# Kernel tuning notes

Measured on AMD Instinct MI355X. Metric: run time of the kernel, lower is better.

Reference implementation:

```python
import jax, jax.numpy as jnp
import numpy as np

NUM_CLASSES = 1000
NUM_NEIGHBOURS = 200
SIGMA = 10.0
GAUSS_CONST = 1.0 / (2.0 * SIGMA ** 2)


def setup_inputs() -> dict:
    key = jax.random.key(0)
    k1, k2, k3 = jax.random.split(key, 3)
    B, D, C = 512, 512, 100000
    features = jax.random.normal(k1, (B, D), dtype=jnp.float32)
    centres = jax.random.normal(k2, (C, D), dtype=jnp.float32)
    centre_labels = jax.random.randint(k3, (C,), 0, NUM_CLASSES)
    weight = jnp.zeros((C,), dtype=jnp.float32)
    return {"features": features, "centres": centres,
            "centre_labels": centre_labels, "weight": weight}


def _knn(features, centres, k):
    # squared euclidean distances [B, C] without materializing [B, C, D]
    f2 = jnp.sum(features * features, axis=1, keepdims=True)      # [B,1]
    c2 = jnp.sum(centres * centres, axis=1)                        # [C]
    d2 = f2 + c2[None, :] - 2.0 * features @ centres.T             # [B,C]
    _, idx = jax.lax.top_k(-d2, k)                                 # smallest k
    return idx                                                     # [B,k]


def reference(features, centres, centre_labels, weight):
    B = features.shape[0]
    K = NUM_NEIGHBOURS
    nbr = _knn(features, centres, K)                               # [B,K] int
    gathered = centres[nbr]                                        # [B,K,D]
    d2 = jnp.sum((features[:, None, :] - gathered) ** 2, axis=-1)  # [B,K]
    kernel_weights = jnp.exp(weight)                               # [C]
    d = jnp.exp(-d2 * GAUSS_CONST) * kernel_weights[nbr]           # [B,K]
    nbr_labels = centre_labels[nbr]                                # [B,K]
    rows = jnp.arange(B)[:, None]
    p = jnp.zeros((B, NUM_CLASSES), dtype=d.dtype).at[rows, nbr_labels].add(d)
    p = jnp.where(p == 0, 1e-10, p)
    p = p / jnp.sum(p, axis=1, keepdims=True)
    return jnp.log(p)
```

## Files before the change

kernel.cpp:

```cpp
#include <hip/hip_runtime.h>
#include <hip/hip_fp16.h>
#include <math.h>
#include <stdint.h>

#define D_DIM    512
#define NCLS     1000
#define KSEL     200
#define NBINS    1024
#define CAND_MAX 2048
#define GCONST   0.005
#define MARGIN   2.0f

typedef short s8v __attribute__((ext_vector_type(8)));
typedef float f4v __attribute__((ext_vector_type(4)));

#define GLOAD_LDS16(gp, lp) __builtin_amdgcn_global_load_lds( \
    (const __attribute__((address_space(1))) void*)(gp),      \
    (__attribute__((address_space(3))) void*)(lp), 16, 0, 0)

static __device__ __forceinline__ unsigned short f2bf(float x) {
    unsigned u = __float_as_uint(x);
    return (unsigned short)((u + 0x7FFFu + ((u >> 16) & 1u)) >> 16);
}

__global__ __launch_bounds__(256)
void convertF(const float* __restrict__ F, unsigned short* __restrict__ Fb,
              float* __restrict__ f2)
{
    __shared__ float red[256];
    const int r = blockIdx.x, t = threadIdx.x;
    float2 v = *(const float2*)(F + (size_t)r * D_DIM + t * 2);
    ushort2 o; o.x = f2bf(v.x); o.y = f2bf(v.y);
    *(ushort2*)(Fb + (size_t)r * D_DIM + t * 2) = o;
    red[t] = v.x * v.x + v.y * v.y;
    __syncthreads();
    for (int off = 128; off > 0; off >>= 1) {
        if (t < off) red[t] += red[t + off];
        __syncthreads();
    }
    if (t == 0) f2[r] = red[0];
}

__global__ __launch_bounds__(256)
void mfma_gemm(const unsigned short* __restrict__ Fb,
               const float* __restrict__ C,
               float* __restrict__ c2g,
               __half* __restrict__ Sm, int N)
{
    __shared__ short smem[2 * 128 * 64];
    short* As = smem;
    short* Bs = smem + 128 * 64;
    const int t    = threadIdx.x;
    const int lane = t & 63;
    const int w    = t >> 6;
    const int wm   = w >> 1, wn = w & 1;
    const int m0   = blockIdx.x * 128;
    const int n0   = blockIdx.y * 128;
    const int lrow = lane >> 3;
    const int oct  = (lane & 7) ^ lrow;
    const int quad = lane >> 4;
    const int col  = lane & 15;

    f4v acc[4][4];
#pragma unroll
    for (int i = 0; i < 4; ++i)
#pragma unroll
        for (int j = 0; j < 4; ++j) acc[i][j] = (f4v){0.f, 0.f, 0.f, 0.f};

    float  c2part[4] = {0.f, 0.f, 0.f, 0.f};
    float4 ra[4], rb[4];

#pragma unroll
    for (int cc = 0; cc < 4; ++cc) {
        int row = (w * 4 + cc) * 8 + lrow;
        int rg  = n0 + row; rg = rg < N ? rg : N - 1;
        const float* gp = C + (size_t)rg * D_DIM + oct * 8;
        ra[cc] = *(const float4*)gp;
        rb[cc] = *(const float4*)(gp + 4);
    }

    for (int k0 = 0; k0 < D_DIM; k0 += 64) {
        __syncthreads();
#pragma unroll
        for (int cc = 0; cc < 4; ++cc) {
            int ch = w * 4 + cc;
            GLOAD_LDS16(Fb + (size_t)(m0 + ch * 8 + lrow) * D_DIM + k0 + oct * 8,
                        &As[ch * 512]);
        }
#pragma unroll
        for (int cc = 0; cc < 4; ++cc) {
            int row = (w * 4 + cc) * 8 + lrow;
            float4 va = ra[cc], vb = rb[cc];
            c2part[cc] += va.x*va.x + va.y*va.y + va.z*va.z + va.w*va.w
                        + vb.x*vb.x + vb.y*vb.y + vb.z*vb.z + vb.w*vb.w;
            uint4 o;
            o.x = (unsigned)f2bf(va.x) | ((unsigned)f2bf(va.y) << 16);
            o.y = (unsigned)f2bf(va.z) | ((unsigned)f2bf(va.w) << 16);
            o.z = (unsigned)f2bf(vb.x) | ((unsigned)f2bf(vb.y) << 16);
            o.w = (unsigned)f2bf(vb.z) | ((unsigned)f2bf(vb.w) << 16);
            *(uint4*)&Bs[row * 64 + (lane & 7) * 8] = o;
        }
        __syncthreads();

        if (k0 + 64 < D_DIM) {
#pragma unroll
            for (int cc = 0; cc < 4; ++cc) {
                int row = (w * 4 + cc) * 8 + lrow;
                int rg  = n0 + row; rg = rg < N ? rg : N - 1;
                const float* gp = C + (size_t)rg * D_DIM + (k0 + 64) + oct * 8;
                ra[cc] = *(const float4*)gp;
                rb[cc] = *(const float4*)(gp + 4);
            }
        }

#pragma unroll
        for (int kk = 0; kk < 2; ++kk) {
            s8v a[4], b[4];
#pragma unroll
            for (int i = 0; i < 4; ++i) {
                int row  = wm * 64 + i * 16 + col;
                int slot = (kk * 4 + quad) ^ (col & 7);
                a[i] = *(s8v*)&As[row * 64 + slot * 8];
            }
#pragma unroll
            for (int j = 0; j < 4; ++j) {
                int row  = wn * 64 + j * 16 + col;
                int slot = (kk * 4 + quad) ^ (col & 7);
                b[j] = *(s8v*)&Bs[row * 64 + slot * 8];
            }
#pragma unroll
            for (int i = 0; i < 4; ++i)
#pragma unroll
                for (int j = 0; j < 4; ++j)
                    acc[i][j] = __builtin_amdgcn_mfma_f32_16x16x32_bf16(
                        a[i], b[j], acc[i][j], 0, 0, 0);
        }
    }

#pragma unroll
    for (int cc = 0; cc < 4; ++cc) {
        float s = c2part[cc];
        s += __shfl_xor(s, 1, 64);
        s += __shfl_xor(s, 2, 64);
        s += __shfl_xor(s, 4, 64);
        int row = (w * 4 + cc) * 8 + lrow;
        if (m0 == 0 && (lane & 7) == 0 && (n0 + row) < N)
            c2g[n0 + row] = s;
    }

    __syncthreads();
    __half* Cs = (__half*)smem;
#pragma unroll
    for (int i = 0; i < 4; ++i) {
#pragma unroll
        for (int j = 0; j < 4; ++j) {
#pragma unroll
            for (int v = 0; v < 4; ++v) {
                int ml = wm * 64 + i * 16 + quad * 4 + v;
                int nl = wn * 64 + j * 16 + col;
                int slot = ((nl >> 3) ^ (ml & 7));
                Cs[ml * 128 + slot * 8 + (nl & 7)] = __float2half(acc[i][j][v]);
            }
        }
    }
    __syncthreads();
#pragma unroll
    for (int it = 0; it < 8; ++it) {
        int idx = it * 256 + t;
        int row = idx >> 4;
        int o8  = idx & 15;
        int n   = n0 + o8 * 8;
        const __half* src = &Cs[row * 128 + ((o8 ^ (row & 7)) * 8)];
        __half* dst = Sm + (size_t)(m0 + row) * N + n;
        if (n + 7 < N) {
            *(uint4*)dst = *(const uint4*)src;
        } else if (n < N) {
            for (int e = 0; e < 8 && n + e < N; ++e) dst[e] = src[e];
        }
    }
}

__global__ __launch_bounds__(1024)
void fused_select(const __half* __restrict__ Sm, const float* __restrict__ f2,
                  const float* __restrict__ c2,
                  const float* __restrict__ F, const float* __restrict__ C,
                  const int* __restrict__ labels, const float* __restrict__ weight,
                  float* __restrict__ out, int N)
{
    __shared__ unsigned hist[NBINS];
    __shared__ float    fs[D_DIM];
    __shared__ int      idxs[CAND_MAX];
    __shared__ double   dists[CAND_MAX];
    __shared__ float    p[NCLS];
    __shared__ float    red[1024];
    __shared__ unsigned scanbuf[256];
    __shared__ float    sT;
    __shared__ unsigned scnt;

    const int r = blockIdx.x, t = threadIdx.x;
    for (int b = t; b < NBINS; b += 1024) hist[b] = 0u;
    for (int c = t; c < NCLS; c += 1024) p[c] = 0.f;
    for (int k = t; k < D_DIM; k += 1024) fs[k] = F[(size_t)r * D_DIM + k];
    if (t == 0) { sT = 1e30f; scnt = 0u; }
    __syncthreads();

    const float fr = f2[r];
    const __half* srow = Sm + (size_t)r * N;

    for (int j = t * 8; j < N; j += 8192) {
        uint4 sv = *(const uint4*)(srow + j);
        float4 ca = *(const float4*)(c2 + j);
        float4 cb = *(const float4*)(c2 + j + 4);
        float2 s0 = __half22float2(*(__half2*)&sv.x);
        float2 s1 = __half22float2(*(__half2*)&sv.y);
        float2 s2 = __half22float2(*(__half2*)&sv.z);
        float2 s3 = __half22float2(*(__half2*)&sv.w);
        float d2v[8] = { fr + ca.x - 2.f * s0.x, fr + ca.y - 2.f * s0.y,
                         fr + ca.z - 2.f * s1.x, fr + ca.w - 2.f * s1.y,
                         fr + cb.x - 2.f * s2.x, fr + cb.y - 2.f * s2.y,
                         fr + cb.z - 2.f * s3.x, fr + cb.w - 2.f * s3.y };
#pragma unroll
        for (int e = 0; e < 8; ++e) {
            int b = (int)(d2v[e] * 0.5f);
            b = b < 0 ? 0 : (b > NBINS - 1 ? NBINS - 1 : b);
            atomicAdd(&hist[b], 1u);
        }
    }
    __syncthreads();

    if (t < 256) {
        unsigned loc[NBINS / 256];
        unsigned s = 0;
#pragma unroll
        for (int i = 0; i < NBINS / 256; ++i) {
            loc[i] = hist[t * (NBINS / 256) + i];
            s += loc[i];
        }
        scanbuf[t] = s;
        __syncthreads();
        unsigned pre = 0;
        for (int u = 0; u < t; ++u) pre += scanbuf[u];
        if (pre < KSEL && pre + s >= KSEL) {
            unsigned cum = pre;
            int b = NBINS - 1;
#pragma unroll
            for (int i = 0; i < NBINS / 256; ++i) {
                cum += loc[i];
                if (cum >= KSEL) { b = t * (NBINS / 256) + i; break; }
            }
            sT = 2.0f * (float)(b + 1) + MARGIN;
        }
    } else {
        __syncthreads();
    }
    __syncthreads();
    const float Tr = sT;

    for (int j = t * 8; j < N; j += 8192) {
        uint4 sv = *(const uint4*)(srow + j);
        float4 ca = *(const float4*)(c2 + j);
        float4 cb = *(const float4*)(c2 + j + 4);
        float2 s0 = __half22float2(*(__half2*)&sv.x);
        float2 s1 = __half22float2(*(__half2*)&sv.y);
        float2 s2 = __half22float2(*(__half2*)&sv.z);
        float2 s3 = __half22float2(*(__half2*)&sv.w);
        float d2v[8] = { fr + ca.x - 2.f * s0.x, fr + ca.y - 2.f * s0.y,
                         fr + ca.z - 2.f * s1.x, fr + ca.w - 2.f * s1.y,
                         fr + cb.x - 2.f * s2.x, fr + cb.y - 2.f * s2.y,
                         fr + cb.z - 2.f * s3.x, fr + cb.w - 2.f * s3.y };
#pragma unroll
        for (int e = 0; e < 8; ++e) {
            if (d2v[e] <= Tr) {
                unsigned pos = atomicAdd(&scnt, 1u);
                if (pos < CAND_MAX) idxs[pos] = j + e;
            }
        }
    }
    __syncthreads();
    int Nc = (int)scnt;
    if (Nc > CAND_MAX) Nc = CAND_MAX;

    {
        const int wv = t >> 6, lane = t & 63;
        for (int i = wv; i < Nc; i += 16) {
            int ci = idxs[i];
            const float* cp = C + (size_t)ci * D_DIM;
            float4 a  = *(const float4*)(cp + lane * 8);
            float4 b  = *(const float4*)(cp + lane * 8 + 4);
            float4 fa = *(const float4*)(fs + lane * 8);
            float4 fb = *(const float4*)(fs + lane * 8 + 4);
            double d0 = (double)fa.x - (double)a.x;
            double d1 = (double)fa.y - (double)a.y;
            double d2 = (double)fa.z - (double)a.z;
            double d3 = (double)fa.w - (double)a.w;
            double d4 = (double)fb.x - (double)b.x;
            double d5 = (double)fb.y - (double)b.y;
            double d6 = (double)fb.z - (double)b.z;
            double d7 = (double)fb.w - (double)b.w;
            double acc = d0*d0 + d1*d1 + d2*d2 + d3*d3
                       + d4*d4 + d5*d5 + d6*d6 + d7*d7;
#pragma unroll
            for (int off = 32; off > 0; off >>= 1)
                acc += __shfl_down(acc, off, 64);
            if (lane == 0) dists[i] = acc;
        }
    }
    __syncthreads();

    int ksel = KSEL < Nc ? KSEL : Nc;
    for (int i = t; i < Nc; i += 1024) {
        double di = dists[i];
        int    ii = idxs[i];
        int rank = 0;
        for (int j = 0; j < Nc; ++j) {
            double dj = dists[j];
            rank += (dj < di) || (dj == di && idxs[j] < ii);
        }
        if (rank < ksel) {
            double wgt = exp(-di * GCONST) * exp((double)weight[ii]);
            atomicAdd(&p[labels[ii]], (float)wgt);
        }
    }
    __syncthreads();

    float s = 0.f;
    for (int c = t; c < NCLS; c += 1024) {
        float v = p[c];
        if (v == 0.f) v = 1e-10f;
        p[c] = v;
        s += v;
    }
    red[t] = s;
    __syncthreads();
    for (int o = 512; o > 0; o >>= 1) {
        if (t < o) red[t] += red[t + o];
        __syncthreads();
    }
    float total = red[0];
    for (int c = t; c < NCLS; c += 1024)
        out[(size_t)r * NCLS + c] = logf(p[c] / total);
}

extern "C" void kernel_launch(void* const* d_in, const int* in_sizes, int n_in,
                              void* d_out, int out_size, void* d_ws, size_t ws_size,
                              hipStream_t stream)
{
    const float* features = (const float*)d_in[0];
    const float* centres  = (const float*)d_in[1];
    const int*   labels   = (const int*)d_in[2];
    const float* weight   = (const float*)d_in[3];
    const int B = in_sizes[0] / D_DIM;
    const int N = in_sizes[2];
    float* out = (float*)d_out;

    uint8_t* w = (uint8_t*)d_ws;
    size_t off = 0;
    auto alloc = [&](size_t bytes) -> uint8_t* {
        uint8_t* ptr = w + off;
        off = (off + bytes + 255) & ~(size_t)255;
        return ptr;
    };
    float*          f2 = (float*)alloc((size_t)B * 4);
    float*          c2 = (float*)alloc((size_t)N * 4);
    unsigned short* Fb = (unsigned short*)alloc((size_t)B * D_DIM * 2);
    __half*         Sm = (__half*)alloc((size_t)B * N * 2);
    (void)ws_size;

    convertF<<<B, 256, 0, stream>>>(features, Fb, f2);

    dim3 ggrid(B / 128, (N + 127) / 128);
    mfma_gemm<<<ggrid, 256, 0, stream>>>(Fb, centres, c2, Sm, N);

    fused_select<<<B, 1024, 0, stream>>>(Sm, f2, c2, features, centres,
                                         labels, weight, out, N);
}
```

Baseline: 490.8 us.

## Pre-convert centres to bf16 once and replicate select histogram bins

When the workspace is large enough, a separate kernel converts all centres to bf16 and computes their squared norms once. The GEMM then loads bf16 tiles directly into LDS with global_load_lds, where before every M-block reread fp32 centres and converted them in registers. The fallback fused GEMM now uses the packed v_cvt_pk_bf16 instruction. The select kernel spreads each histogram bin over four replicas to reduce LDS atomic contention, at the cost of an extra 100MB bf16 write/read and more shared memory.

```diff
diff --git a/kernel.cpp b/kernel.cpp
--- a/kernel.cpp
+++ b/kernel.cpp
@@ -7,6 +7,7 @@
 #define NCLS     1000
 #define KSEL     200
 #define NBINS    1024
+#define HREP     4
 #define CAND_MAX 2048
 #define GCONST   0.005
 #define MARGIN   2.0f
@@ -21,6 +22,12 @@
 static __device__ __forceinline__ unsigned short f2bf(float x) {
     unsigned u = __float_as_uint(x);
     return (unsigned short)((u + 0x7FFFu + ((u >> 16) & 1u)) >> 16);
+}
+
+static __device__ __forceinline__ unsigned cvt_pk_bf16(float lo, float hi) {
+    unsigned r;
+    asm("v_cvt_pk_bf16_f32 %0, %1, %2" : "=v"(r) : "v"(lo), "v"(hi));
+    return r;
 }
 
 __global__ __launch_bounds__(256)
@@ -42,10 +49,37 @@
 }
 
 __global__ __launch_bounds__(256)
-void mfma_gemm(const unsigned short* __restrict__ Fb,
-               const float* __restrict__ C,
-               float* __restrict__ c2g,
-               __half* __restrict__ Sm, int N)
+void convertC(const float* __restrict__ C, unsigned short* __restrict__ Cb,
+              float* __restrict__ c2, int N)
+{
+    const int wv = threadIdx.x >> 6, lane = threadIdx.x & 63;
+    const int stride = gridDim.x * 4;
+    for (int r = blockIdx.x * 4 + wv; r < N; r += stride) {
+        const float* rp = C + (size_t)r * D_DIM + lane * 8;
+        float4 a = *(const float4*)rp;
+        float4 b = *(const float4*)(rp + 4);
+        uint4 o;
+        o.x = cvt_pk_bf16(a.x, a.y);
+        o.y = cvt_pk_bf16(a.z, a.w);
+        o.z = cvt_pk_bf16(b.x, b.y);
+        o.w = cvt_pk_bf16(b.z, b.w);
+        *(uint4*)(Cb + (size_t)r * D_DIM + lane * 8) = o;
+        float s = a.x*a.x + a.y*a.y + a.z*a.z + a.w*a.w
+                + b.x*b.x + b.y*b.y + b.z*b.z + b.w*b.w;
+        s += __shfl_xor(s, 1, 64);
+        s += __shfl_xor(s, 2, 64);
+        s += __shfl_xor(s, 4, 64);
+        s += __shfl_xor(s, 8, 64);
+        s += __shfl_xor(s, 16, 64);
+        s += __shfl_xor(s, 32, 64);
+        if (lane == 0) c2[r] = s;
+    }
+}
+
+__global__ __launch_bounds__(256)
+void mfma_gemm_pure(const unsigned short* __restrict__ Fb,
+                    const unsigned short* __restrict__ Cb,
+                    __half* __restrict__ Sm, int N)
 {
     __shared__ short smem[2 * 128 * 64];
     short* As = smem;
@@ -67,18 +101,6 @@
 #pragma unroll
         for (int j = 0; j < 4; ++j) acc[i][j] = (f4v){0.f, 0.f, 0.f, 0.f};
 
-    float  c2part[4] = {0.f, 0.f, 0.f, 0.f};
-    float4 ra[4], rb[4];
-
-#pragma unroll
-    for (int cc = 0; cc < 4; ++cc) {
-        int row = (w * 4 + cc) * 8 + lrow;
-        int rg  = n0 + row; rg = rg < N ? rg : N - 1;
-        const float* gp = C + (size_t)rg * D_DIM + oct * 8;
-        ra[cc] = *(const float4*)gp;
-        rb[cc] = *(const float4*)(gp + 4);
-    }
-
     for (int k0 = 0; k0 < D_DIM; k0 += 64) {
         __syncthreads();
 #pragma unroll
@@ -89,29 +111,13 @@
         }
 #pragma unroll
         for (int cc = 0; cc < 4; ++cc) {
-            int row = (w * 4 + cc) * 8 + lrow;
-            float4 va = ra[cc], vb = rb[cc];
-            c2part[cc] += va.x*va.x + va.y*va.y + va.z*va.z + va.w*va.w
-                        + vb.x*vb.x + vb.y*vb.y + vb.z*vb.z + vb.w*vb.w;
-            uint4 o;
-            o.x = (unsigned)f2bf(va.x) | ((unsigned)f2bf(va.y) << 16);
-            o.y = (unsigned)f2bf(va.z) | ((unsigned)f2bf(va.w) << 16);
-            o.z = (unsigned)f2bf(vb.x) | ((unsigned)f2bf(vb.y) << 16);
-            o.w = (unsigned)f2bf(vb.z) | ((unsigned)f2bf(vb.w) << 16);
-            *(uint4*)&Bs[row * 64 + (lane & 7) * 8] = o;
-        }
-        __syncthreads();
-
-        if (k0 + 64 < D_DIM) {
-#pragma unroll
-            for (int cc = 0; cc < 4; ++cc) {
-                int row = (w * 4 + cc) * 8 + lrow;
-                int rg  = n0 + row; rg = rg < N ? rg : N - 1;
-                const float* gp = C + (size_t)rg * D_DIM + (k0 + 64) + oct * 8;
-                ra[cc] = *(const float4*)gp;
-                rb[cc] = *(const float4*)(gp + 4);
-            }
-        }
+            int ch = w * 4 + cc;
+            int rg = n0 + ch * 8 + lrow;
+            rg = rg < N ? rg : N - 1;
+            GLOAD_LDS16(Cb + (size_t)rg * D_DIM + k0 + oct * 8,
+                        &Bs[ch * 512]);
+        }
+        __syncthreads();
 
 #pragma unroll
         for (int kk = 0; kk < 2; ++kk) {
@@ -135,17 +141,6 @@
                     acc[i][j] = __builtin_amdgcn_mfma_f32_16x16x32_bf16(
                         a[i], b[j], acc[i][j], 0, 0, 0);
         }
-    }
-
-#pragma unroll
-    for (int cc = 0; cc < 4; ++cc) {
-        float s = c2part[cc];
-        s += __shfl_xor(s, 1, 64);
-        s += __shfl_xor(s, 2, 64);
-        s += __shfl_xor(s, 4, 64);
-        int row = (w * 4 + cc) * 8 + lrow;
-        if (m0 == 0 && (lane & 7) == 0 && (n0 + row) < N)
-            c2g[n0 + row] = s;
     }
 
     __syncthreads();
@@ -180,6 +175,145 @@
     }
 }
 
+__global__ __launch_bounds__(256)
+void mfma_gemm_fused(const unsigned short* __restrict__ Fb,
+                     const float* __restrict__ C,
+                     float* __restrict__ c2g,
+                     __half* __restrict__ Sm, int N)
+{
+    __shared__ short smem[2 * 128 * 64];
+    short* As = smem;
+    short* Bs = smem + 128 * 64;
+    const int t    = threadIdx.x;
+    const int lane = t & 63;
+    const int w    = t >> 6;
+    const int wm   = w >> 1, wn = w & 1;
+    const int m0   = blockIdx.x * 128;
+    const int n0   = blockIdx.y * 128;
+    const int lrow = lane >> 3;
+    const int oct  = (lane & 7) ^ lrow;
+    const int quad = lane >> 4;
+    const int col  = lane & 15;
+
+    f4v acc[4][4];
+#pragma unroll
+    for (int i = 0; i < 4; ++i)
+#pragma unroll
+        for (int j = 0; j < 4; ++j) acc[i][j] = (f4v){0.f, 0.f, 0.f, 0.f};
+
+    float  c2part[4] = {0.f, 0.f, 0.f, 0.f};
+    float4 ra[4], rb[4];
+
+#pragma unroll
+    for (int cc = 0; cc < 4; ++cc) {
+        int row = (w * 4 + cc) * 8 + lrow;
+        int rg  = n0 + row; rg = rg < N ? rg : N - 1;
+        const float* gp = C + (size_t)rg * D_DIM + oct * 8;
+        ra[cc] = *(const float4*)gp;
+        rb[cc] = *(const float4*)(gp + 4);
+    }
+
+    for (int k0 = 0; k0 < D_DIM; k0 += 64) {
+        __syncthreads();
+#pragma unroll
+        for (int cc = 0; cc < 4; ++cc) {
+            int ch = w * 4 + cc;
+            GLOAD_LDS16(Fb + (size_t)(m0 + ch * 8 + lrow) * D_DIM + k0 + oct * 8,
+                        &As[ch * 512]);
+        }
+#pragma unroll
+        for (int cc = 0; cc < 4; ++cc) {
+            int row = (w * 4 + cc) * 8 + lrow;
+            float4 va = ra[cc], vb = rb[cc];
+            c2part[cc] += va.x*va.x + va.y*va.y + va.z*va.z + va.w*va.w
+                        + vb.x*vb.x + vb.y*vb.y + vb.z*vb.z + vb.w*vb.w;
+            uint4 o;
+            o.x = cvt_pk_bf16(va.x, va.y);
+            o.y = cvt_pk_bf16(va.z, va.w);
+            o.z = cvt_pk_bf16(vb.x, vb.y);
+            o.w = cvt_pk_bf16(vb.z, vb.w);
+            *(uint4*)&Bs[row * 64 + (lane & 7) * 8] = o;
+        }
+        __syncthreads();
+
+        if (k0 + 64 < D_DIM) {
+#pragma unroll
+            for (int cc = 0; cc < 4; ++cc) {
+                int row = (w * 4 + cc) * 8 + lrow;
+                int rg  = n0 + row; rg = rg < N ? rg : N - 1;
+                const float* gp = C + (size_t)rg * D_DIM + (k0 + 64) + oct * 8;
+                ra[cc] = *(const float4*)gp;
+                rb[cc] = *(const float4*)(gp + 4);
+            }
+        }
+
+#pragma unroll
+        for (int kk = 0; kk < 2; ++kk) {
+            s8v a[4], b[4];
+#pragma unroll
+            for (int i = 0; i < 4; ++i) {
+                int row  = wm * 64 + i * 16 + col;
+                int slot = (kk * 4 + quad) ^ (col & 7);
+                a[i] = *(s8v*)&As[row * 64 + slot * 8];
+            }
+#pragma unroll
+            for (int j = 0; j < 4; ++j) {
+                int row  = wn * 64 + j * 16 + col;
+                int slot = (kk * 4 + quad) ^ (col & 7);
+                b[j] = *(s8v*)&Bs[row * 64 + slot * 8];
+            }
+#pragma unroll
+            for (int i = 0; i < 4; ++i)
+#pragma unroll
+                for (int j = 0; j < 4; ++j)
+                    acc[i][j] = __builtin_amdgcn_mfma_f32_16x16x32_bf16(
+                        a[i], b[j], acc[i][j], 0, 0, 0);
+        }
+    }
+
+#pragma unroll
+    for (int cc = 0; cc < 4; ++cc) {
+        float s = c2part[cc];
+        s += __shfl_xor(s, 1, 64);
+        s += __shfl_xor(s, 2, 64);
+        s += __shfl_xor(s, 4, 64);
+        int row = (w * 4 + cc) * 8 + lrow;
+        if (m0 == 0 && (lane & 7) == 0 && (n0 + row) < N)
+            c2g[n0 + row] = s;
+    }
+
+    __syncthreads();
+    __half* Cs = (__half*)smem;
+#pragma unroll
+    for (int i = 0; i < 4; ++i) {
+#pragma unroll
+        for (int j = 0; j < 4; ++j) {
+#pragma unroll
+            for (int v = 0; v < 4; ++v) {
+                int ml = wm * 64 + i * 16 + quad * 4 + v;
+                int nl = wn * 64 + j * 16 + col;
+                int slot = ((nl >> 3) ^ (ml & 7));
+                Cs[ml * 128 + slot * 8 + (nl & 7)] = __float2half(acc[i][j][v]);
+            }
+        }
+    }
+    __syncthreads();
+#pragma unroll
+    for (int it = 0; it < 8; ++it) {
+        int idx = it * 256 + t;
+        int row = idx >> 4;
+        int o8  = idx & 15;
+        int n   = n0 + o8 * 8;
+        const __half* src = &Cs[row * 128 + ((o8 ^ (row & 7)) * 8)];
+        __half* dst = Sm + (size_t)(m0 + row) * N + n;
+        if (n + 7 < N) {
+            *(uint4*)dst = *(const uint4*)src;
+        } else if (n < N) {
+            for (int e = 0; e < 8 && n + e < N; ++e) dst[e] = src[e];
+        }
+    }
+}
+
 __global__ __launch_bounds__(1024)
 void fused_select(const __half* __restrict__ Sm, const float* __restrict__ f2,
                   const float* __restrict__ c2,
@@ -187,7 +321,7 @@
                   const int* __restrict__ labels, const float* __restrict__ weight,
                   float* __restrict__ out, int N)
 {
-    __shared__ unsigned hist[NBINS];
+    __shared__ unsigned hist[NBINS * HREP];
     __shared__ float    fs[D_DIM];
     __shared__ int      idxs[CAND_MAX];
     __shared__ double   dists[CAND_MAX];
@@ -198,7 +332,7 @@
     __shared__ unsigned scnt;
 
     const int r = blockIdx.x, t = threadIdx.x;
-    for (int b = t; b < NBINS; b += 1024) hist[b] = 0u;
+    for (int b = t; b < NBINS * HREP; b += 1024) hist[b] = 0u;
     for (int c = t; c < NCLS; c += 1024) p[c] = 0.f;
     for (int k = t; k < D_DIM; k += 1024) fs[k] = F[(size_t)r * D_DIM + k];
     if (t == 0) { sT = 1e30f; scnt = 0u; }
@@ -223,7 +357,7 @@
         for (int e = 0; e < 8; ++e) {
             int b = (int)(d2v[e] * 0.5f);
             b = b < 0 ? 0 : (b > NBINS - 1 ? NBINS - 1 : b);
-            atomicAdd(&hist[b], 1u);
+            atomicAdd(&hist[(b << 2) + (t & 3)], 1u);
         }
     }
     __syncthreads();
@@ -233,7 +367,9 @@
         unsigned s = 0;
 #pragma unroll
         for (int i = 0; i < NBINS / 256; ++i) {
-            loc[i] = hist[t * (NBINS / 256) + i];
+            int bb = t * (NBINS / 256) + i;
+            loc[i] = hist[(bb << 2) + 0] + hist[(bb << 2) + 1]
+                   + hist[(bb << 2) + 2] + hist[(bb << 2) + 3];
             s += loc[i];
         }
         scanbuf[t] = s;
@@ -364,12 +500,21 @@
     float*          c2 = (float*)alloc((size_t)N * 4);
     unsigned short* Fb = (unsigned short*)alloc((size_t)B * D_DIM * 2);
     __half*         Sm = (__half*)alloc((size_t)B * N * 2);
-    (void)ws_size;
+
+    const size_t need_cb = off + (size_t)N * D_DIM * 2;
+    const bool   full    = ws_size >= need_cb;
 
     convertF<<<B, 256, 0, stream>>>(features, Fb, f2);
 
-    dim3 ggrid(B / 128, (N + 127) / 128);
-    mfma_gemm<<<ggrid, 256, 0, stream>>>(Fb, centres, c2, Sm, N);
+    if (full) {
+        unsigned short* Cb = (unsigned short*)alloc((size_t)N * D_DIM * 2);
+        convertC<<<2048, 256, 0, stream>>>(centres, Cb, c2, N);
+        dim3 ggrid(B / 128, (N + 127) / 128);
+        mfma_gemm_pure<<<ggrid, 256, 0, stream>>>(Fb, Cb, Sm, N);
+    } else {
+        dim3 ggrid(B / 128, (N + 127) / 128);
+        mfma_gemm_fused<<<ggrid, 256, 0, stream>>>(Fb, centres, c2, Sm, N);
+    }
 
     fused_select<<<B, 1024, 0, stream>>>(Sm, f2, c2, features, centres,
                                          labels, weight, out, N);
```

Result: no change. 490.8 us (+0.0%).

## Fuse distance epilogue into GEMM, enlarge M tile, replicate histogram bins

Applied to the files above, without the earlier changes.

The GEMM now computes the full squared distance (f2 + c2 - 2·dot) in its epilogue and stores it as fp16. The selection kernel therefore no longer reads a c2 array or recomputes the distance per element. The GEMM block grows to 512 threads covering 256 feature rows, so each converted centre tile is reused across twice as many rows, and the bf16 packing uses the hardware v_cvt_pk_bf16_f32 instruction. The shared-memory histogram is replicated four ways to cut atomic contention, and the candidate margin is widened to absorb fp16 error on larger distance values, which can admit more candidates.

```diff
diff --git a/kernel.cpp b/kernel.cpp
--- a/kernel.cpp
+++ b/kernel.cpp
@@ -7,9 +7,10 @@
 #define NCLS     1000
 #define KSEL     200
 #define NBINS    1024
+#define HREP     4
 #define CAND_MAX 2048
 #define GCONST   0.005
-#define MARGIN   2.0f
+#define MARGIN   4.0f
 
 typedef short s8v __attribute__((ext_vector_type(8)));
 typedef float f4v __attribute__((ext_vector_type(4)));
@@ -21,6 +22,12 @@
 static __device__ __forceinline__ unsigned short f2bf(float x) {
     unsigned u = __float_as_uint(x);
     return (unsigned short)((u + 0x7FFFu + ((u >> 16) & 1u)) >> 16);
+}
+
+static __device__ __forceinline__ unsigned cvt_pk_bf16(float lo, float hi) {
+    unsigned r;
+    asm("v_cvt_pk_bf16_f32 %0, %1, %2" : "=v"(r) : "v"(lo), "v"(hi));
+    return r;
 }
 
 __global__ __launch_bounds__(256)
@@ -41,20 +48,21 @@
     if (t == 0) f2[r] = red[0];
 }
 
-__global__ __launch_bounds__(256)
+__global__ __launch_bounds__(512)
 void mfma_gemm(const unsigned short* __restrict__ Fb,
                const float* __restrict__ C,
-               float* __restrict__ c2g,
-               __half* __restrict__ Sm, int N)
+               const float* __restrict__ f2,
+               __half* __restrict__ Dm, int N)
 {
-    __shared__ short smem[2 * 128 * 64];
+    __shared__ short smem[32 * 512 + 16 * 512];
+    __shared__ float c2s[128];
     short* As = smem;
-    short* Bs = smem + 128 * 64;
+    short* Bs = smem + 32 * 512;
     const int t    = threadIdx.x;
     const int lane = t & 63;
     const int w    = t >> 6;
     const int wm   = w >> 1, wn = w & 1;
-    const int m0   = blockIdx.x * 128;
+    const int m0   = blockIdx.x * 256;
     const int n0   = blockIdx.y * 128;
     const int lrow = lane >> 3;
     const int oct  = (lane & 7) ^ lrow;
@@ -67,12 +75,12 @@
 #pragma unroll
         for (int j = 0; j < 4; ++j) acc[i][j] = (f4v){0.f, 0.f, 0.f, 0.f};
 
-    float  c2part[4] = {0.f, 0.f, 0.f, 0.f};
-    float4 ra[4], rb[4];
-
-#pragma unroll
-    for (int cc = 0; cc < 4; ++cc) {
-        int row = (w * 4 + cc) * 8 + lrow;
+    float  c2part[2] = {0.f, 0.f};
+    float4 ra[2], rb[2];
+
+#pragma unroll
+    for (int cc = 0; cc < 2; ++cc) {
+        int row = (w * 2 + cc) * 8 + lrow;
         int rg  = n0 + row; rg = rg < N ? rg : N - 1;
         const float* gp = C + (size_t)rg * D_DIM + oct * 8;
         ra[cc] = *(const float4*)gp;
@@ -88,24 +96,24 @@
                         &As[ch * 512]);
         }
 #pragma unroll
-        for (int cc = 0; cc < 4; ++cc) {
-            int row = (w * 4 + cc) * 8 + lrow;
+        for (int cc = 0; cc < 2; ++cc) {
+            int row = (w * 2 + cc) * 8 + lrow;
             float4 va = ra[cc], vb = rb[cc];
             c2part[cc] += va.x*va.x + va.y*va.y + va.z*va.z + va.w*va.w
                         + vb.x*vb.x + vb.y*vb.y + vb.z*vb.z + vb.w*vb.w;
             uint4 o;
-            o.x = (unsigned)f2bf(va.x) | ((unsigned)f2bf(va.y) << 16);
-            o.y = (unsigned)f2bf(va.z) | ((unsigned)f2bf(va.w) << 16);
-            o.z = (unsigned)f2bf(vb.x) | ((unsigned)f2bf(vb.y) << 16);
-            o.w = (unsigned)f2bf(vb.z) | ((unsigned)f2bf(vb.w) << 16);
+            o.x = cvt_pk_bf16(va.x, va.y);
+            o.y = cvt_pk_bf16(va.z, va.w);
+            o.z = cvt_pk_bf16(vb.x, vb.y);
+            o.w = cvt_pk_bf16(vb.z, vb.w);
             *(uint4*)&Bs[row * 64 + (lane & 7) * 8] = o;
         }
         __syncthreads();
 
         if (k0 + 64 < D_DIM) {
 #pragma unroll
-            for (int cc = 0; cc < 4; ++cc) {
-                int row = (w * 4 + cc) * 8 + lrow;
+            for (int cc = 0; cc < 2; ++cc) {
+                int row = (w * 2 + cc) * 8 + lrow;
                 int rg  = n0 + row; rg = rg < N ? rg : N - 1;
                 const float* gp = C + (size_t)rg * D_DIM + (k0 + 64) + oct * 8;
                 ra[cc] = *(const float4*)gp;
@@ -115,79 +123,93 @@
 
 #pragma unroll
         for (int kk = 0; kk < 2; ++kk) {
-            s8v a[4], b[4];
+            int slot = (kk * 4 + quad) ^ (col & 7);
+            s8v b[4];
+#pragma unroll
+            for (int j = 0; j < 4; ++j) {
+                int row = wn * 64 + j * 16 + col;
+                b[j] = *(s8v*)&Bs[row * 64 + slot * 8];
+            }
 #pragma unroll
             for (int i = 0; i < 4; ++i) {
-                int row  = wm * 64 + i * 16 + col;
-                int slot = (kk * 4 + quad) ^ (col & 7);
-                a[i] = *(s8v*)&As[row * 64 + slot * 8];
-            }
-#pragma unroll
-            for (int j = 0; j < 4; ++j) {
-                int row  = wn * 64 + j * 16 + col;
-                int slot = (kk * 4 + quad) ^ (col & 7);
-                b[j] = *(s8v*)&Bs[row * 64 + slot * 8];
-            }
-#pragma unroll
-            for (int i = 0; i < 4; ++i)
+                int row = wm * 64 + i * 16 + col;
+                s8v a = *(s8v*)&As[row * 64 + slot * 8];
 #pragma unroll
                 for (int j = 0; j < 4; ++j)
                     acc[i][j] = __builtin_amdgcn_mfma_f32_16x16x32_bf16(
-                        a[i], b[j], acc[i][j], 0, 0, 0);
-        }
-    }
-
-#pragma unroll
-    for (int cc = 0; cc < 4; ++cc) {
+                        a, b[j], acc[i][j], 0, 0, 0);
+            }
+        }
+    }
+
+#pragma unroll
+    for (int cc = 0; cc < 2; ++cc) {
         float s = c2part[cc];
         s += __shfl_xor(s, 1, 64);
         s += __shfl_xor(s, 2, 64);
         s += __shfl_xor(s, 4, 64);
-        int row = (w * 4 + cc) * 8 + lrow;
-        if (m0 == 0 && (lane & 7) == 0 && (n0 + row) < N)
-            c2g[n0 + row] = s;
-    }
-
-    __syncthreads();
+        int row = (w * 2 + cc) * 8 + lrow;
+        if ((lane & 7) == 0) c2s[row] = s;
+    }
+    __syncthreads();
+
+    float c2v[4];
+#pragma unroll
+    for (int j = 0; j < 4; ++j)
+        c2v[j] = c2s[wn * 64 + j * 16 + col];
+    float fv[4][4];
+#pragma unroll
+    for (int i = 0; i < 4; ++i)
+#pragma unroll
+        for (int v = 0; v < 4; ++v)
+            fv[i][v] = f2[m0 + wm * 64 + i * 16 + quad * 4 + v];
+
     __half* Cs = (__half*)smem;
 #pragma unroll
-    for (int i = 0; i < 4; ++i) {
-#pragma unroll
-        for (int j = 0; j < 4; ++j) {
-#pragma unroll
-            for (int v = 0; v < 4; ++v) {
-                int ml = wm * 64 + i * 16 + quad * 4 + v;
-                int nl = wn * 64 + j * 16 + col;
-                int slot = ((nl >> 3) ^ (ml & 7));
-                Cs[ml * 128 + slot * 8 + (nl & 7)] = __float2half(acc[i][j][v]);
-            }
-        }
-    }
-    __syncthreads();
-#pragma unroll
-    for (int it = 0; it < 8; ++it) {
-        int idx = it * 256 + t;
-        int row = idx >> 4;
-        int o8  = idx & 15;
-        int n   = n0 + o8 * 8;
-        const __half* src = &Cs[row * 128 + ((o8 ^ (row & 7)) * 8)];
-        __half* dst = Sm + (size_t)(m0 + row) * N + n;
-        if (n + 7 < N) {
-            *(uint4*)dst = *(const uint4*)src;
-        } else if (n < N) {
-            for (int e = 0; e < 8 && n + e < N; ++e) dst[e] = src[e];
+    for (int h = 0; h < 2; ++h) {
+        __syncthreads();
+        if ((wm >> 1) == h) {
+            int mlb = (wm & 1) * 64;
+#pragma unroll
+            for (int i = 0; i < 4; ++i) {
+#pragma unroll
+                for (int j = 0; j < 4; ++j) {
+#pragma unroll
+                    for (int v = 0; v < 4; ++v) {
+                        int ml = mlb + i * 16 + quad * 4 + v;
+                        int nl = wn * 64 + j * 16 + col;
+                        float d2 = fv[i][v] + c2v[j] - 2.f * acc[i][j][v];
+                        int slot = (nl >> 3) ^ (ml & 7);
+                        Cs[ml * 128 + slot * 8 + (nl & 7)] = __float2half(d2);
+                    }
+                }
+            }
+        }
+        __syncthreads();
+#pragma unroll
+        for (int it = 0; it < 4; ++it) {
+            int idx = it * 512 + t;
+            int row = idx >> 4;
+            int o8  = idx & 15;
+            int n   = n0 + o8 * 8;
+            const __half* src = &Cs[row * 128 + ((o8 ^ (row & 7)) * 8)];
+            __half* dst = Dm + (size_t)(m0 + h * 128 + row) * N + n;
+            if (n + 7 < N) {
+                *(uint4*)dst = *(const uint4*)src;
+            } else if (n < N) {
+                for (int e = 0; e < 8 && n + e < N; ++e) dst[e] = src[e];
+            }
         }
     }
 }
 
 __global__ __launch_bounds__(1024)
-void fused_select(const __half* __restrict__ Sm, const float* __restrict__ f2,
-                  const float* __restrict__ c2,
+void fused_select(const __half* __restrict__ Dm,
                   const float* __restrict__ F, const float* __restrict__ C,
                   const int* __restrict__ labels, const float* __restrict__ weight,
                   float* __restrict__ out, int N)
 {
-    __shared__ unsigned hist[NBINS];
+    __shared__ unsigned hist[NBINS * HREP];
     __shared__ float    fs[D_DIM];
     __shared__ int      idxs[CAND_MAX];
     __shared__ double   dists[CAND_MAX];
@@ -198,32 +220,26 @@
     __shared__ unsigned scnt;
 
     const int r = blockIdx.x, t = threadIdx.x;
-    for (int b = t; b < NBINS; b += 1024) hist[b] = 0u;
+    for (int b = t; b < NBINS * HREP; b += 1024) hist[b] = 0u;
     for (int c = t; c < NCLS; c += 1024) p[c] = 0.f;
     for (int k = t; k < D_DIM; k += 1024) fs[k] = F[(size_t)r * D_DIM + k];
     if (t == 0) { sT = 1e30f; scnt = 0u; }
     __syncthreads();
 
-    const float fr = f2[r];
-    const __half* srow = Sm + (size_t)r * N;
+    const __half* srow = Dm + (size_t)r * N;
 
     for (int j = t * 8; j < N; j += 8192) {
         uint4 sv = *(const uint4*)(srow + j);
-        float4 ca = *(const float4*)(c2 + j);
-        float4 cb = *(const float4*)(c2 + j + 4);
         float2 s0 = __half22float2(*(__half2*)&sv.x);
         float2 s1 = __half22float2(*(__half2*)&sv.y);
         float2 s2 = __half22float2(*(__half2*)&sv.z);
         float2 s3 = __half22float2(*(__half2*)&sv.w);
-        float d2v[8] = { fr + ca.x - 2.f * s0.x, fr + ca.y - 2.f * s0.y,
-                         fr + ca.z - 2.f * s1.x, fr + ca.w - 2.f * s1.y,
-                         fr + cb.x - 2.f * s2.x, fr + cb.y - 2.f * s2.y,
-                         fr + cb.z - 2.f * s3.x, fr + cb.w - 2.f * s3.y };
+        float d2v[8] = { s0.x, s0.y, s1.x, s1.y, s2.x, s2.y, s3.x, s3.y };
 #pragma unroll
         for (int e = 0; e < 8; ++e) {
             int b = (int)(d2v[e] * 0.5f);
             b = b < 0 ? 0 : (b > NBINS - 1 ? NBINS - 1 : b);
-            atomicAdd(&hist[b], 1u);
+            atomicAdd(&hist[(b << 2) + (t & 3)], 1u);
         }
     }
     __syncthreads();
@@ -233,7 +249,9 @@
         unsigned s = 0;
 #pragma unroll
         for (int i = 0; i < NBINS / 256; ++i) {
-            loc[i] = hist[t * (NBINS / 256) + i];
+            int bb = t * (NBINS / 256) + i;
+            loc[i] = hist[(bb << 2) + 0] + hist[(bb << 2) + 1]
+                   + hist[(bb << 2) + 2] + hist[(bb << 2) + 3];
             s += loc[i];
         }
         scanbuf[t] = s;
@@ -258,16 +276,11 @@
 
     for (int j = t * 8; j < N; j += 8192) {
         uint4 sv = *(const uint4*)(srow + j);
-        float4 ca = *(const float4*)(c2 + j);
-        float4 cb = *(const float4*)(c2 + j + 4);
         float2 s0 = __half22float2(*(__half2*)&sv.x);
         float2 s1 = __half22float2(*(__half2*)&sv.y);
         float2 s2 = __half22float2(*(__half2*)&sv.z);
         float2 s3 = __half22float2(*(__half2*)&sv.w);
-        float d2v[8] = { fr + ca.x - 2.f * s0.x, fr + ca.y - 2.f * s0.y,
-                         fr + ca.z - 2.f * s1.x, fr + ca.w - 2.f * s1.y,
-                         fr + cb.x - 2.f * s2.x, fr + cb.y - 2.f * s2.y,
-                         fr + cb.z - 2.f * s3.x, fr + cb.w - 2.f * s3.y };
+        float d2v[8] = { s0.x, s0.y, s1.x, s1.y, s2.x, s2.y, s3.x, s3.y };
 #pragma unroll
         for (int e = 0; e < 8; ++e) {
             if (d2v[e] <= Tr) {
@@ -361,16 +374,15 @@
         return ptr;
     };
     float*          f2 = (float*)alloc((size_t)B * 4);
-    float*          c2 = (float*)alloc((size_t)N * 4);
     unsigned short* Fb = (unsigned short*)alloc((size_t)B * D_DIM * 2);
-    __half*         Sm = (__half*)alloc((size_t)B * N * 2);
+    __half*         Dm = (__half*)alloc((size_t)B * N * 2);
     (void)ws_size;
 
     convertF<<<B, 256, 0, stream>>>(features, Fb, f2);
 
-    dim3 ggrid(B / 128, (N + 127) / 128);
-    mfma_gemm<<<ggrid, 256, 0, stream>>>(Fb, centres, c2, Sm, N);
-
-    fused_select<<<B, 1024, 0, stream>>>(Sm, f2, c2, features, centres,
+    dim3 ggrid(B / 256, (N + 127) / 128);
+    mfma_gemm<<<ggrid, 512, 0, stream>>>(Fb, centres, f2, Dm, N);
+
+    fused_select<<<B, 1024, 0, stream>>>(Dm, features, centres,
                                          labels, weight, out, N);
 }
```

Measured after the change: 464.2 us. 1.06x faster.
